# Kernel optimization log

Hardware: AMD Instinct MI355X
Metric: run time of the kernel (lower is better)

The kernel has to match this reference:

```python
import jax, jax.numpy as jnp
import numpy as np

HEADS = 8
D_MODEL = 512

def setup_inputs() -> dict:
    key = jax.random.key(0)
    ks = jax.random.split(key, 7)
    t, w, h, b = 8, 14, 14, 8
    seq = t * w * h + 1  # 1569, includes CLS token
    q = jax.random.normal(ks[0], (seq, b, D_MODEL), jnp.float32)
    k = jax.random.normal(ks[1], (seq, b, D_MODEL), jnp.float32)
    value = jax.random.normal(ks[2], (seq, b, D_MODEL), jnp.float32)
    in_proj_weight = jax.random.normal(ks[3], (3 * D_MODEL, D_MODEL), jnp.float32) * (D_MODEL ** -0.5)
    in_proj_bias = jax.random.normal(ks[4], (3 * D_MODEL,), jnp.float32) * 0.02
    out_w = jax.random.normal(ks[5], (D_MODEL, D_MODEL), jnp.float32) * (D_MODEL ** -0.5)
    out_b = jax.random.normal(ks[6], (D_MODEL,), jnp.float32) * 0.02
    return {"q": q, "k": k, "value": value,
            "in_proj_weight": in_proj_weight, "in_proj_bias": in_proj_bias,
            "out_w": out_w, "out_b": out_b, "t": t, "w": w, "h": h}

def _sdpa(q, k, v):
    # scaled dot-product attention over batched 3D tensors [B, L, dh]
    temp = q.shape[-1] ** 0.5
    scores = jnp.einsum('bqd,bkd->bqk', q, k) / temp
    a = jax.nn.softmax(scores, axis=-1)  # softmax over dim=2 == last dim
    return jnp.einsum('bqk,bkd->bqd', a, v), a

def reference(q, k, value, in_proj_weight, in_proj_bias, out_w, out_b, t, w, h):
    seq, b, c = q.shape
    H, dh, wh = HEADS, c // HEADS, w * h
    q_cls = q[:1]          # [1, b, c] passed through untouched
    x = q[1:]              # [t*wh, b, c]
    qkv = x @ in_proj_weight.T + in_proj_bias  # fused QKV proj
    qq, kk, vv = qkv[..., :c], qkv[..., c:2 * c], qkv[..., 2 * c:]
    to5 = lambda z: z.reshape(t, wh, b, H, dh)
    # spatial stage: batch = (H, b, t), attend over wh
    q_s = to5(qq).transpose(3, 2, 0, 1, 4).reshape(H * b * t, wh, dh)
    k_s = to5(kk).transpose(3, 2, 0, 1, 4).reshape(H * b * t, wh, dh)
    v_s = to5(vv).transpose(3, 2, 0, 1, 4).reshape(H * b * t, wh, dh)
    out_s, attn = _sdpa(q_s, k_s, v_s)
    # temporal stage: batch = (H, b, wh), attend over t; V comes from spatial output
    v_t = out_s.reshape(H, b, t, wh, dh).transpose(0, 1, 3, 2, 4).reshape(H * b * wh, t, dh)
    q_t = to5(qq).transpose(3, 2, 1, 0, 4).reshape(H * b * wh, t, dh)
    k_t = to5(kk).transpose(3, 2, 1, 0, 4).reshape(H * b * wh, t, dh)
    out_t, _ = _sdpa(q_t, k_t, v_t)
    # back to [t*wh, b, c]
    out = out_t.reshape(H, b, wh, t, dh).transpose(3, 2, 1, 0, 4).reshape(t * wh, b, c)
    out = out @ out_w.T + out_b
    return jnp.concatenate([q_cls, out], axis=0), attn
```

## Files before the change

### kernel.cpp

```cpp
#include <hip/hip_runtime.h>
#include <cstdint>
#include <cstddef>

typedef __bf16 bf16;
typedef __bf16 bf16x8 __attribute__((ext_vector_type(8)));
typedef __bf16 bf16x4 __attribute__((ext_vector_type(4)));
typedef float  f32x4  __attribute__((ext_vector_type(4)));

#define MFMA16(a, b, c) __builtin_amdgcn_mfma_f32_16x16x32_bf16(a, b, c, 0, 0, 0)

__device__ __forceinline__ void gl2lds16(const bf16* g, bf16* l) {
  __builtin_amdgcn_global_load_lds(
      (const __attribute__((address_space(1))) void*)g,
      (__attribute__((address_space(3))) void*)l, 16, 0, 0);
}

__device__ __forceinline__ void cvt4(const float* __restrict__ s, bf16* __restrict__ d) {
  f32x4 v = *(const f32x4*)s;
  bf16x4 o;
  o[0] = (bf16)v[0]; o[1] = (bf16)v[1]; o[2] = (bf16)v[2]; o[3] = (bf16)v[3];
  *(bf16x4*)d = o;
}

__global__ __launch_bounds__(256) void prep_kernel(
    const float* __restrict__ q, const float* __restrict__ win,
    const float* __restrict__ wout, float* __restrict__ out0,
    bf16* __restrict__ xb, bf16* __restrict__ wqb, bf16* __restrict__ wob) {
  long u = (long)blockIdx.x * 256 + threadIdx.x;
  const long NX4 = 1605632, NWQ4 = 196608, NWO4 = 65536, NQC4 = 1024;
  if (u < NX4) { cvt4(q + 4096 + u * 4, xb + u * 4); return; }
  u -= NX4;
  if (u < NWQ4) { cvt4(win + u * 4, wqb + u * 4); return; }
  u -= NWQ4;
  if (u < NWO4) { cvt4(wout + u * 4, wob + u * 4); return; }
  u -= NWO4;
  if (u < NQC4) { *(f32x4*)(out0 + u * 4) = *(const f32x4*)(q + u * 4); }
}

__global__ __launch_bounds__(256) void gemm_bt(
    const bf16* __restrict__ A, const bf16* __restrict__ Bm,
    const float* __restrict__ bias, float* __restrict__ Cf,
    int N, int K, long coff) {
  __shared__ bf16 As[128 * 64];
  __shared__ bf16 Bs[128 * 64];
  const int tid = threadIdx.x;
  const int wid = tid >> 6, lane = tid & 63;
  const int lr = lane & 15, lg = lane >> 4;

  const int nwg = gridDim.x * gridDim.y;
  const int orig = blockIdx.y * gridDim.x + blockIdx.x;
  const int cpx = nwg >> 3;
  const int swz = (orig & 7) * cpx + (orig >> 3);
  const int m0 = (swz / gridDim.x) * 128;
  const int n0 = (swz % gridDim.x) * 128;

  const int wr = wid >> 1, wc = wid & 1;
  const int slot = lane & 7, r8 = lane >> 3;
  const int chunk = slot ^ r8;
  const int x7 = lr & 7;

  f32x4 acc[4][4] = {};

  for (int kt = 0; kt < K; kt += 64) {
    __syncthreads();
#pragma unroll
    for (int j = 0; j < 4; ++j) {
      int blk = wid * 4 + j;
      int row = blk * 8 + r8;
      gl2lds16(A + (size_t)(m0 + row) * K + kt + chunk * 8, As + blk * 512);
      gl2lds16(Bm + (size_t)(n0 + row) * K + kt + chunk * 8, Bs + blk * 512);
    }
    __syncthreads();

#pragma unroll
    for (int kk = 0; kk < 2; ++kk) {
      bf16x8 af[4], bfr[4];
#pragma unroll
      for (int m = 0; m < 4; ++m)
        af[m] = *(const bf16x8*)(As + (wr * 64 + m * 16 + lr) * 64 +
                                 (((kk * 4 + lg) ^ x7) * 8));
#pragma unroll
      for (int n = 0; n < 4; ++n)
        bfr[n] = *(const bf16x8*)(Bs + (wc * 64 + n * 16 + lr) * 64 +
                                  (((kk * 4 + lg) ^ x7) * 8));
#pragma unroll
      for (int m = 0; m < 4; ++m)
#pragma unroll
        for (int n = 0; n < 4; ++n)
          acc[m][n] = MFMA16(af[m], bfr[n], acc[m][n]);
    }
  }

#pragma unroll
  for (int m = 0; m < 4; ++m) {
    int row = m0 + wr * 64 + m * 16 + lg * 4;
#pragma unroll
    for (int n = 0; n < 4; ++n) {
      int col = n0 + wc * 64 + n * 16 + lr;
      float bv = bias[col];
#pragma unroll
      for (int i = 0; i < 4; ++i)
        __builtin_nontemporal_store(
            acc[m][n][i] + bv, Cf + coff + (size_t)(row + i) * N + col);
    }
  }
}

__global__ __launch_bounds__(1024) void spatial_fused(
    const bf16* __restrict__ xb, const bf16* __restrict__ wqb,
    const float* __restrict__ bin, bf16* __restrict__ Qh,
    bf16* __restrict__ Kh, float* __restrict__ attn_out,
    bf16* __restrict__ outs) {
  __shared__ bf16 Kl[224 * 72];
  __shared__ bf16 Vt[64 * 232];
  __shared__ bf16 RB[40768];
  bf16* const Xs  = RB;
  bf16* const Wss = RB + 13312;
  bf16* const Qb  = RB + 25600;
  bf16* const StgB = RB;

  const int tid = threadIdx.x;
  const int wid = tid >> 6, lane = tid & 63;
  const int lr = lane & 15, lg = lane >> 4;
  const int batch = blockIdx.x;
  const int h = batch >> 6;
  const int bb = (batch >> 3) & 7;
  const int ti = batch & 7;

  { int d = tid >> 4, r = 208 + (tid & 15); Vt[d * 232 + r] = (bf16)0.f; }

  const int r8 = lane >> 3, slot = lane & 7;
  const int chunk = slot ^ r8;
  const int x7 = lr & 7;

  const int qg = wid >> 2, ng = wid & 3;
  const int nfb = ng * 3;
  f32x4 acc[4][3] = {};

  for (int kt = 0; kt < 512; kt += 64) {
    __syncthreads();
#pragma unroll
    for (int t = 0; t < 4; ++t) {
      int task = wid + t * 16;
      if (task < 26) {
        int row = task * 8 + r8;
        int xr = row > 195 ? 195 : row;
        gl2lds16(xb + ((size_t)(ti * 196 + xr) * 8 + bb) * 512 + kt +
                     chunk * 8,
                 Xs + task * 512);
      } else if (task < 50) {
        int j = task - 26;
        int strip = j >> 3;
        int wrow = strip * 512 + h * 64 + (j & 7) * 8 + r8;
        gl2lds16(wqb + (size_t)wrow * 512 + kt + chunk * 8, Wss + j * 512);
      }
    }
    __syncthreads();
#pragma unroll
    for (int kk = 0; kk < 2; ++kk) {
      const int xoff = ((kk * 4 + lg) ^ x7) * 8;
      bf16x8 af[4];
#pragma unroll
      for (int qi = 0; qi < 4; ++qi)
        af[qi] = *(const bf16x8*)(Xs + ((qg * 4 + qi) * 16 + lr) * 64 + xoff);
#pragma unroll
      for (int nj = 0; nj < 3; ++nj) {
        bf16x8 bfr = *(const bf16x8*)(Wss + ((nfb + nj) * 16 + lr) * 64 + xoff);
#pragma unroll
        for (int qi = 0; qi < 4; ++qi)
          acc[qi][nj] = MFMA16(af[qi], bfr, acc[qi][nj]);
      }
    }
  }

#pragma unroll
  for (int qi = 0; qi < 4; ++qi) {
    const int qtg = qg * 4 + qi;
    if (qtg < 13) {
#pragma unroll
      for (int nj = 0; nj < 3; ++nj) {
        const int nf = nfb + nj;
        const int strip = nf >> 2;
        float bv = bin[strip * 512 + h * 64 + (nf & 3) * 16 + lr];
        f32x4 a = acc[qi][nj];
#pragma unroll
        for (int i = 0; i < 4; ++i) a[i] += bv;
        if (strip == 0) {
          bf16* qb = Qb + qtg * 1152;
#pragma unroll
          for (int i = 0; i < 4; ++i)
            qb[(lg * 4 + i) * 72 + (nf & 3) * 16 + lr] = (bf16)a[i];
        } else if (strip == 1) {
#pragma unroll
          for (int i = 0; i < 4; ++i)
            Kl[(qtg * 16 + lg * 4 + i) * 72 + (nf & 3) * 16 + lr] =
                (bf16)a[i];
        } else {
          union { bf16x4 h4; uint2 u; } pk;
          pk.h4[0] = (bf16)a[0]; pk.h4[1] = (bf16)a[1];
          pk.h4[2] = (bf16)a[2]; pk.h4[3] = (bf16)a[3];
          int d = (nf & 3) * 16 + lr;
          *(uint2*)&Vt[d * 232 + qtg * 16 + lg * 4] = pk.u;
        }
      }
    }
  }
  __syncthreads();

  const int qt = wid;
  bf16x8 aq[2];
  if (qt < 13) {
    const bf16* qb = Qb + qt * 1152;
#pragma unroll
    for (int kk = 0; kk < 2; ++kk)
      aq[kk] = *(const bf16x8*)(qb + lr * 72 + kk * 32 + lg * 8);
    bf16* slabQ = Qh + (size_t)batch * 12544;
    bf16* slabK = Kh + (size_t)batch * 12544;
    const int erow = lane >> 3, eseg = lane & 7;
#pragma unroll
    for (int t = 0; t < 2; ++t) {
      int row = qt * 16 + t * 8 + erow;
      if (row < 196) {
        *(bf16x8*)(slabQ + row * 64 + eseg * 8) =
            *(const bf16x8*)(qb + (t * 8 + erow) * 72 + eseg * 8);
        *(bf16x8*)(slabK + row * 64 + eseg * 8) =
            *(const bf16x8*)(Kl + row * 72 + eseg * 8);
      }
    }
  }
  __syncthreads();

  if (qt < 13) {
    const int q = qt * 16 + lr;

    f32x4 s[14] = {};
    __builtin_amdgcn_s_setprio(1);
#pragma unroll
    for (int nn = 0; nn < 14; ++nn) {
      const int krow = nn * 16 + lr;
      bf16x8 bk0 = *(const bf16x8*)&Kl[krow * 72 + lg * 8];
      bf16x8 bk1 = *(const bf16x8*)&Kl[krow * 72 + 32 + lg * 8];
      s[nn] = MFMA16(bk0, aq[0], s[nn]);
      s[nn] = MFMA16(bk1, aq[1], s[nn]);
    }
    __builtin_amdgcn_s_setprio(0);

#pragma unroll
    for (int nn = 0; nn < 14; ++nn) {
      bool pad = (nn * 16 + lg * 4 >= 196);
#pragma unroll
      for (int i = 0; i < 4; ++i)
        s[nn][i] = pad ? -1e30f : s[nn][i] * 0.125f;
    }

    float v = -1e30f;
#pragma unroll
    for (int nn = 0; nn < 14; ++nn)
#pragma unroll
      for (int i = 0; i < 4; ++i) v = fmaxf(v, s[nn][i]);
    v = fmaxf(v, __shfl_xor(v, 16));
    v = fmaxf(v, __shfl_xor(v, 32));
    float sum = 0.f;
#pragma unroll
    for (int nn = 0; nn < 14; ++nn)
#pragma unroll
      for (int i = 0; i < 4; ++i) {
        float e = __expf(s[nn][i] - v);
        s[nn][i] = e;
        sum += e;
      }
    sum += __shfl_xor(sum, 16);
    sum += __shfl_xor(sum, 32);
    const float rinv = 1.f / sum;

    bf16* const tile = StgB + qt * 3136;
    const int low = lr + 32 * (lg & 1);
    const int high = low + 16;
    const bool hiN = (lg >> 1) != 0;
    f32x4 o[4] = {};
#pragma unroll
    for (int kb = 0; kb < 7; ++kb) {
      uint32_t px[2], py[2];
#pragma unroll
      for (int t = 0; t < 2; ++t) {
        const int nn = 2 * kb + t;
        f32x4 sv;
#pragma unroll
        for (int i = 0; i < 4; ++i) sv[i] = s[nn][i] * rinv;
        union { bf16x4 h4; uint2 u; } pk;
        pk.h4[0] = (bf16)sv[0]; pk.h4[1] = (bf16)sv[1];
        pk.h4[2] = (bf16)sv[2]; pk.h4[3] = (bf16)sv[3];
        int kbase = nn * 16 + lg * 4;
        if (kbase < 196)
          *(uint2*)((char*)tile + lr * 392 + kbase * 2) = pk.u;
        px[t] = pk.u.x; py[t] = pk.u.y;
      }
      uint32_t a0x = __shfl((int)px[0], low);
      uint32_t a0y = __shfl((int)py[0], low);
      uint32_t a1x = __shfl((int)px[1], low);
      uint32_t a1y = __shfl((int)py[1], low);
      uint32_t b0x = __shfl((int)px[0], high);
      uint32_t b0y = __shfl((int)py[0], high);
      uint32_t b1x = __shfl((int)px[1], high);
      uint32_t b1y = __shfl((int)py[1], high);
      union { uint32_t u[4]; bf16x8 h8; } pa;
      pa.u[0] = hiN ? a1x : a0x;
      pa.u[1] = hiN ? a1y : a0y;
      pa.u[2] = hiN ? b1x : b0x;
      pa.u[3] = hiN ? b1y : b0y;
      __builtin_amdgcn_s_setprio(1);
#pragma unroll
      for (int nd = 0; nd < 4; ++nd) {
        bf16x8 vb = *(const bf16x8*)&Vt[(nd * 16 + lr) * 232 + kb * 32 + lg * 8];
        o[nd] = MFMA16(pa.h8, vb, o[nd]);
      }
      __builtin_amdgcn_s_setprio(0);
    }

    {
      const int hb8 = batch >> 3;
#pragma unroll
      for (int i = 0; i < 4; ++i) {
        int p = qt * 16 + lg * 4 + i;
        if (p < 196) {
#pragma unroll
          for (int nd = 0; nd < 4; ++nd) {
            int d = nd * 16 + lr;
            outs[(((size_t)(hb8 * 196 + p)) * 8 + ti) * 64 + d] =
                (bf16)o[nd][i];
          }
        }
      }
    }

    {
      const int vbytes = (qt == 12) ? 3136 : 12544;
      char* dst = (char*)(attn_out + (size_t)batch * 38416 + qt * 3136);
      const char* src = (const char*)tile;
#pragma unroll
      for (int j = 0; j < 13; ++j) {
        int x = j * 1024 + lane * 16;
        if (x < vbytes) {
          uint2 u = *(const uint2*)(src + (x >> 1));
          union { uint32_t b; float f; } c0, c1, c2, c3;
          c0.b = (u.x & 0xffffu) << 16; c1.b = u.x & 0xffff0000u;
          c2.b = (u.y & 0xffffu) << 16; c3.b = u.y & 0xffff0000u;
          f32x4 ov; ov[0] = c0.f; ov[1] = c1.f; ov[2] = c2.f; ov[3] = c3.f;
          *(f32x4*)(dst + x) = ov;
        }
      }
    }
  }
}

__global__ __launch_bounds__(256) void temporal_attn(
    const bf16* __restrict__ Qh, const bf16* __restrict__ Kh,
    const bf16* __restrict__ outs, bf16* __restrict__ outt) {
  __shared__ bf16 Ql[4][8][72];
  __shared__ bf16 Kc[4][8][72];
  __shared__ bf16 Vl[4][8][64];
  __shared__ float Ps[4][8][8];

  const int tid = threadIdx.x, wid = tid >> 6, lane = tid & 63;
  const int batch = blockIdx.x * 4 + wid;
  const int p = batch % 196;
  const int hb = batch / 196;
  const int bb = hb & 7, h = hb >> 3;

  const int ri = lane >> 3;
  const int c8 = lane & 7;
  {
    size_t so = ((size_t)(h * 64 + bb * 8 + ri)) * 12544 + p * 64 + c8 * 8;
    *(bf16x8*)&Ql[wid][ri][c8 * 8] = *(const bf16x8*)(Qh + so);
    *(bf16x8*)&Kc[wid][ri][c8 * 8] = *(const bf16x8*)(Kh + so);
    *(bf16x8*)&Vl[wid][ri][c8 * 8] =
        *(const bf16x8*)(outs + ((size_t)batch * 8 + ri) * 64 + c8 * 8);
  }
  __syncthreads();

  float s = 0.f;
#pragma unroll
  for (int d = 0; d < 64; d += 8) {
    bf16x8 qv = *(const bf16x8*)&Ql[wid][ri][d];
    bf16x8 kv = *(const bf16x8*)&Kc[wid][c8][d];
#pragma unroll
    for (int e = 0; e < 8; ++e) s += (float)qv[e] * (float)kv[e];
  }
  s *= 0.125f;
  float mxv = s;
#pragma unroll
  for (int d2 = 1; d2 < 8; d2 <<= 1) mxv = fmaxf(mxv, __shfl_xor(mxv, d2));
  float e = __expf(s - mxv);
  float sum = e;
#pragma unroll
  for (int d2 = 1; d2 < 8; d2 <<= 1) sum += __shfl_xor(sum, d2);
  Ps[wid][ri][c8] = e / sum;
  __syncthreads();

  const int d = lane;
#pragma unroll
  for (int ii = 0; ii < 8; ++ii) {
    float o = 0.f;
#pragma unroll
    for (int j = 0; j < 8; ++j) o += Ps[wid][ii][j] * (float)Vl[wid][j][d];
    outt[((size_t)(ii * 196 + p) * 8 + bb) * 512 + h * 64 + d] = (bf16)o;
  }
}

extern "C" void kernel_launch(void* const* d_in, const int* in_sizes, int n_in,
                              void* d_out, int out_size, void* d_ws,
                              size_t ws_size, hipStream_t stream) {
  (void)in_sizes; (void)n_in; (void)out_size; (void)ws_size;
  const float* q    = (const float*)d_in[0];
  const float* win  = (const float*)d_in[3];
  const float* bin  = (const float*)d_in[4];
  const float* wout = (const float*)d_in[5];
  const float* bout = (const float*)d_in[6];
  float* out0 = (float*)d_out;
  float* attn = out0 + 6426624L;

  bf16* Qh   = (bf16*)d_ws;
  bf16* Kh   = Qh + 6422528L;
  bf16* outs = Kh + 6422528L;
  bf16* outt = outs + 6422528L;
  bf16* wob  = outt + 6422528L;
  bf16* xb   = wob + 262144L;

  bf16* wqb = (bf16*)(out0 + 4096);

  prep_kernel<<<7300, 256, 0, stream>>>(q, win, wout, out0, xb, wqb, wob);
  spatial_fused<<<512, 1024, 0, stream>>>(xb, wqb, bin, Qh, Kh, attn, outs);
  temporal_attn<<<3136, 256, 0, stream>>>(Qh, Kh, outs, outt);
  gemm_bt<<<dim3(4, 98), 256, 0, stream>>>(outt, wob, bout, out0, 512, 512,
                                           4096);
}
```

Measured before the change: 89.50 us.

## Load QKV projection MFMA operands directly from global memory instead of LDS staging

The in-kernel QKV projection inside spatial_fused no longer stages X and weight tiles into shared memory with global_load_lds and two barriers per k-step. Each lane now reads its bf16x8 MFMA fragments straight from global memory through precomputed row pointers, and the k-loop is unrolled by 4. This removes the per-iteration __syncthreads and the LDS round trip. In exchange, operand reuse across waves now depends on the caches, and each wave issues more global loads, some of them redundant.

```diff
diff --git a/kernel.cpp b/kernel.cpp
--- a/kernel.cpp
+++ b/kernel.cpp
@@ -114,9 +114,7 @@
   __shared__ bf16 Kl[224 * 72];
   __shared__ bf16 Vt[64 * 232];
   __shared__ bf16 RB[40768];
-  bf16* const Xs  = RB;
-  bf16* const Wss = RB + 13312;
-  bf16* const Qb  = RB + 25600;
+  bf16* const Qb  = RB;
   bf16* const StgB = RB;
 
   const int tid = threadIdx.x;
@@ -129,48 +127,39 @@
 
   { int d = tid >> 4, r = 208 + (tid & 15); Vt[d * 232 + r] = (bf16)0.f; }
 
-  const int r8 = lane >> 3, slot = lane & 7;
-  const int chunk = slot ^ r8;
-  const int x7 = lr & 7;
-
   const int qg = wid >> 2, ng = wid & 3;
   const int nfb = ng * 3;
+
+  const bf16* xp[4];
+#pragma unroll
+  for (int qi = 0; qi < 4; ++qi) {
+    int p = qg * 64 + qi * 16 + lr;
+    if (p > 195) p = 195;
+    xp[qi] = xb + ((size_t)(ti * 196 + p) * 8 + bb) * 512;
+  }
+  const bf16* wp[3];
+#pragma unroll
+  for (int nj = 0; nj < 3; ++nj) {
+    int nf = nfb + nj;
+    wp[nj] = wqb +
+             (size_t)((nf >> 2) * 512 + h * 64 + (nf & 3) * 16 + lr) * 512;
+  }
+
   f32x4 acc[4][3] = {};
-
-  for (int kt = 0; kt < 512; kt += 64) {
-    __syncthreads();
-#pragma unroll
-    for (int t = 0; t < 4; ++t) {
-      int task = wid + t * 16;
-      if (task < 26) {
-        int row = task * 8 + r8;
-        int xr = row > 195 ? 195 : row;
-        gl2lds16(xb + ((size_t)(ti * 196 + xr) * 8 + bb) * 512 + kt +
-                     chunk * 8,
-                 Xs + task * 512);
-      } else if (task < 50) {
-        int j = task - 26;
-        int strip = j >> 3;
-        int wrow = strip * 512 + h * 64 + (j & 7) * 8 + r8;
-        gl2lds16(wqb + (size_t)wrow * 512 + kt + chunk * 8, Wss + j * 512);
-      }
-    }
-    __syncthreads();
-#pragma unroll
-    for (int kk = 0; kk < 2; ++kk) {
-      const int xoff = ((kk * 4 + lg) ^ x7) * 8;
-      bf16x8 af[4];
+#pragma unroll 4
+  for (int kt = 0; kt < 512; kt += 32) {
+    bf16x8 af[4], bfr[3];
+#pragma unroll
+    for (int qi = 0; qi < 4; ++qi)
+      af[qi] = *(const bf16x8*)(xp[qi] + kt + lg * 8);
+#pragma unroll
+    for (int nj = 0; nj < 3; ++nj)
+      bfr[nj] = *(const bf16x8*)(wp[nj] + kt + lg * 8);
+#pragma unroll
+    for (int nj = 0; nj < 3; ++nj)
 #pragma unroll
       for (int qi = 0; qi < 4; ++qi)
-        af[qi] = *(const bf16x8*)(Xs + ((qg * 4 + qi) * 16 + lr) * 64 + xoff);
-#pragma unroll
-      for (int nj = 0; nj < 3; ++nj) {
-        bf16x8 bfr = *(const bf16x8*)(Wss + ((nfb + nj) * 16 + lr) * 64 + xoff);
-#pragma unroll
-        for (int qi = 0; qi < 4; ++qi)
-          acc[qi][nj] = MFMA16(af[qi], bfr, acc[qi][nj]);
-      }
-    }
+        acc[qi][nj] = MFMA16(af[qi], bfr[nj], acc[qi][nj]);
   }
 
 #pragma unroll
```

New measurement: 153.1 us. 1.71x slower.
